# Kernel optimization log

Measured on AMD Instinct MI355X. Metric: run time of the kernel, lower is better.

The kernel has to match this reference:

```python
import jax, jax.numpy as jnp
import numpy as np

N_BITS = 8
QMAX = 2 ** (N_BITS - 1) - 1  # 127 for int8 symmetric
EPS = 1e-8


def fake_quant(x, axis):
    """Symmetric per-slice (row/col) dynamic fake quantization with STE-compatible form."""
    amax = jnp.max(jnp.abs(x), axis=axis, keepdims=True)
    scale = jnp.maximum(amax, EPS) / QMAX
    q = jnp.clip(jnp.round(x / scale), -QMAX - 1, QMAX) * scale
    return q


def setup_inputs() -> dict:
    key = jax.random.key(0)
    k1, k2 = jax.random.split(key)
    inputs1 = jax.random.normal(k1, (2, 16, 2048, 128), dtype=jnp.float32)
    inputs2 = jax.random.normal(k2, (2, 16, 128, 2048), dtype=jnp.float32)
    return {"inputs1": inputs1, "inputs2": inputs2}


def reference(inputs1, inputs2):
    # input1: row-wise (axes=-1) quant; input2: axes=-1 (module default); output: row-wise
    q1 = fake_quant(inputs1, axis=-1)
    q2 = fake_quant(inputs2, axis=-1)
    out = jnp.matmul(q1, q2)  # [B, H, S, S]
    return fake_quant(out, axis=-1)
```

## Files before the change

kernel.cpp:

```cpp
#include <hip/hip_runtime.h>
#include <hip/hip_bf16.h>
#include <cstdint>

#define QMAXF 127.0f
#define EPSQ 1e-8f

typedef __bf16 bf16x8 __attribute__((ext_vector_type(8)));
typedef float f32x4 __attribute__((ext_vector_type(4)));

static constexpr int BB = 32;
static constexpr int MM = 2048;
static constexpr int KK = 128;
static constexpr int NN = 2048;

static constexpr size_t OFF_Q1   = 0;
static constexpr size_t OFF_Q2T  = OFF_Q1  + (size_t)BB*MM*KK*2;
static constexpr size_t OFF_S1   = OFF_Q2T + (size_t)BB*NN*KK*2;
static constexpr size_t OFF_S2   = OFF_S1  + (size_t)BB*MM*4;

__global__ __launch_bounds__(256) void quant_rows128(const float* __restrict__ x,
                                                     unsigned short* __restrict__ q,
                                                     float* __restrict__ s1) {
    int wave = threadIdx.x >> 6, lane = threadIdx.x & 63;
    int row = blockIdx.x * 4 + wave;
    const float2* xr = reinterpret_cast<const float2*>(x) + (size_t)row * 64;
    float2 v = xr[lane];
    float a = fmaxf(fabsf(v.x), fabsf(v.y));
#pragma unroll
    for (int m = 32; m; m >>= 1) a = fmaxf(a, __shfl_xor(a, m));
    float scale = fmaxf(a, EPSQ) / QMAXF;
    float i0 = fminf(fmaxf(rintf(v.x / scale), -128.f), 127.f);
    float i1 = fminf(fmaxf(rintf(v.y / scale), -128.f), 127.f);
    __bf16 h0 = (__bf16)i0, h1 = (__bf16)i1;
    ushort2 st;
    st.x = *reinterpret_cast<unsigned short*>(&h0);
    st.y = *reinterpret_cast<unsigned short*>(&h1);
    reinterpret_cast<ushort2*>(q + (size_t)row * 128)[lane ^ ((row & 7) << 2)] = st;
    if (lane == 0) s1[row] = scale;
}

__global__ __launch_bounds__(256) void amax_rows2048(const float* __restrict__ x,
                                                     float* __restrict__ s2) {
    int row = blockIdx.x;
    const float4* xr = reinterpret_cast<const float4*>(x) + (size_t)row * 512;
    int t = threadIdx.x;
    float4 v0 = xr[t], v1 = xr[t + 256];
    float a = fmaxf(fmaxf(fmaxf(fabsf(v0.x), fabsf(v0.y)), fmaxf(fabsf(v0.z), fabsf(v0.w))),
                    fmaxf(fmaxf(fabsf(v1.x), fabsf(v1.y)), fmaxf(fabsf(v1.z), fabsf(v1.w))));
#pragma unroll
    for (int m = 32; m; m >>= 1) a = fmaxf(a, __shfl_xor(a, m));
    __shared__ float red[4];
    if ((t & 63) == 0) red[t >> 6] = a;
    __syncthreads();
    if (t == 0) {
        float m0 = fmaxf(fmaxf(red[0], red[1]), fmaxf(red[2], red[3]));
        s2[row] = fmaxf(m0, EPSQ) / QMAXF;
    }
}

__global__ __launch_bounds__(256) void quant_transpose(const float* __restrict__ x,
                                                       const float* __restrict__ s2,
                                                       unsigned short* __restrict__ q2t) {
    int b = blockIdx.x >> 5;
    int n0 = (blockIdx.x & 31) * 64;
    __shared__ unsigned short lds[64][136];
    int t = threadIdx.x;
    int rr = t >> 4, cc = t & 15;
#pragma unroll
    for (int p = 0; p < 8; ++p) {
        int k = p * 16 + rr;
        float s = s2[b * 128 + k];
        const float4* src = reinterpret_cast<const float4*>(x + ((size_t)b * 128 + k) * 2048 + n0);
        float4 v = src[cc];
        float f[4] = {v.x, v.y, v.z, v.w};
#pragma unroll
        for (int e = 0; e < 4; ++e) {
            float iq = fminf(fmaxf(rintf(f[e] / s), -128.f), 127.f);
            __bf16 h = (__bf16)(iq * s);
            lds[cc * 4 + e][k] = *reinterpret_cast<unsigned short*>(&h);
        }
    }
    __syncthreads();
    int nl = t >> 2, seg = t & 3;
    int sw = nl & 7;
    uint4* dstrow = reinterpret_cast<uint4*>(q2t + ((size_t)b * 2048 + n0 + nl) * 128);
#pragma unroll
    for (int j = 0; j < 4; ++j)
        dstrow[(seg * 4 + j) ^ sw] = *reinterpret_cast<const uint4*>(&lds[nl][seg * 32 + j * 8]);
}

__global__ __launch_bounds__(256, 2) void gemm_fused(const unsigned short* __restrict__ qa,
                                                     const unsigned short* __restrict__ qbt,
                                                     const float* __restrict__ s1,
                                                     float* __restrict__ out) {
    int id = blockIdx.x;
    int nid = (id & 7) * 64 + (id >> 3);
    int b = nid >> 4, mt = nid & 15;

    __shared__ unsigned short Bt[2][16384];
    __shared__ float rowAmax[128], sOsc[128], sQs[128], sS1[128];

    int tid = threadIdx.x, wave = tid >> 6, lane = tid & 63;
    if (tid < 128) {
        rowAmax[tid] = 0.f;
        sS1[tid] = s1[b * 2048 + mt * 128 + tid];
    }

    {
        const char* Ag = (const char*)(qa + (size_t)(b * 16 + mt) * 16384);
        const char* Bg = (const char*)(qbt + (size_t)(b * 16) * 16384);
        char* lA = (char*)&Bt[1][0];
        char* lB = (char*)&Bt[0][0];
#pragma unroll
        for (int i = 0; i < 8; ++i) {
            int off = i * 4096 + wave * 1024;
            __builtin_amdgcn_global_load_lds(
                (const __attribute__((address_space(1))) uint32_t*)(Ag + off + lane * 16),
                (__attribute__((address_space(3))) uint32_t*)(lA + off), 16, 0, 0);
            __builtin_amdgcn_global_load_lds(
                (const __attribute__((address_space(1))) uint32_t*)(Bg + off + lane * 16),
                (__attribute__((address_space(3))) uint32_t*)(lB + off), 16, 0, 0);
        }
    }
    __syncthreads();

    int wm = wave >> 1, wn = wave & 1;
    int lr = lane & 15, lg = lane >> 4;
    int swz = (lr & 7) << 3;

    bf16x8 afr[4][4];
#pragma unroll
    for (int ks = 0; ks < 4; ++ks)
#pragma unroll
        for (int mi = 0; mi < 4; ++mi)
            afr[ks][mi] = *reinterpret_cast<const bf16x8*>(
                &Bt[1][(wm * 64 + mi * 16 + lr) * 128 + ((ks * 32 + lg * 8) ^ swz)]);
    __syncthreads();

    size_t ob = (size_t)b * 2048 * 2048;
    float rmax[4] = {0.f, 0.f, 0.f, 0.f};

    for (int it = 0; it < 16; ++it) {
        int cur = it & 1;
        if (it < 15) {
            const char* Bg = (const char*)(qbt + (size_t)(b * 16 + it + 1) * 16384);
            char* lB = (char*)&Bt[cur ^ 1][0];
#pragma unroll
            for (int i = 0; i < 8; ++i) {
                int off = i * 4096 + wave * 1024;
                __builtin_amdgcn_global_load_lds(
                    (const __attribute__((address_space(1))) uint32_t*)(Bg + off + lane * 16),
                    (__attribute__((address_space(3))) uint32_t*)(lB + off), 16, 0, 0);
            }
        }

        f32x4 acc[4][4];
#pragma unroll
        for (int mi = 0; mi < 4; ++mi)
#pragma unroll
            for (int ni = 0; ni < 4; ++ni) {
                f32x4 z = {0.f, 0.f, 0.f, 0.f};
                acc[mi][ni] = z;
            }
#pragma unroll
        for (int ks = 0; ks < 4; ++ks) {
            int kb = (ks * 32 + lg * 8) ^ swz;
            bf16x8 bfr[4];
#pragma unroll
            for (int ni = 0; ni < 4; ++ni)
                bfr[ni] = *reinterpret_cast<const bf16x8*>(&Bt[cur][(wn * 64 + ni * 16 + lr) * 128 + kb]);
#pragma unroll
            for (int mi = 0; mi < 4; ++mi)
#pragma unroll
                for (int ni = 0; ni < 4; ++ni)
                    acc[mi][ni] = __builtin_amdgcn_mfma_f32_16x16x32_bf16(bfr[ni], afr[ks][mi], acc[mi][ni], 0, 0, 0);
        }
#pragma unroll
        for (int mi = 0; mi < 4; ++mi)
#pragma unroll
            for (int ni = 0; ni < 4; ++ni)
#pragma unroll
                for (int r = 0; r < 4; ++r)
                    rmax[mi] = fmaxf(rmax[mi], fabsf(acc[mi][ni][r]));
        __syncthreads();
    }

#pragma unroll
    for (int mi = 0; mi < 4; ++mi) {
        float v = rmax[mi];
        v = fmaxf(v, __shfl_xor(v, 16));
        v = fmaxf(v, __shfl_xor(v, 32));
        if (lg == 0) {
            int row = wm * 64 + mi * 16 + lr;
            atomicMax(reinterpret_cast<unsigned*>(&rowAmax[row]), __float_as_uint(v));
        }
    }
    __syncthreads();
    if (tid < 128) {
        float am = rowAmax[tid] * sS1[tid];
        float osc = fmaxf(am, EPSQ) / QMAXF;
        sOsc[tid] = osc;
        sQs[tid] = sS1[tid] / osc;
    }
    __syncthreads();

    const unsigned short* Bimg = qbt + (size_t)b * 16 * 16384;
    for (int nt = 0; nt < 16; ++nt) {
        f32x4 acc[4][4];
#pragma unroll
        for (int mi = 0; mi < 4; ++mi)
#pragma unroll
            for (int ni = 0; ni < 4; ++ni) {
                f32x4 z = {0.f, 0.f, 0.f, 0.f};
                acc[mi][ni] = z;
            }
#pragma unroll
        for (int ks = 0; ks < 4; ++ks) {
            int kb = (ks * 32 + lg * 8) ^ swz;
            bf16x8 bfr[4];
#pragma unroll
            for (int ni = 0; ni < 4; ++ni)
                bfr[ni] = *reinterpret_cast<const bf16x8*>(
                    &Bimg[(size_t)(nt * 128 + wn * 64 + ni * 16 + lr) * 128 + kb]);
#pragma unroll
            for (int mi = 0; mi < 4; ++mi)
#pragma unroll
                for (int ni = 0; ni < 4; ++ni)
                    acc[mi][ni] = __builtin_amdgcn_mfma_f32_16x16x32_bf16(bfr[ni], afr[ks][mi], acc[mi][ni], 0, 0, 0);
        }
#pragma unroll
        for (int mi = 0; mi < 4; ++mi) {
            int row = wm * 64 + mi * 16 + lr;
            float qs = sQs[row], osc = sOsc[row];
            size_t rowoff = ob + (size_t)(mt * 128 + row) * 2048 + nt * 128 + wn * 64 + lg * 4;
#pragma unroll
            for (int ni = 0; ni < 4; ++ni) {
                f32x4 qv;
                qv[0] = fminf(fmaxf(rintf(acc[mi][ni][0] * qs), -128.f), 127.f) * osc;
                qv[1] = fminf(fmaxf(rintf(acc[mi][ni][1] * qs), -128.f), 127.f) * osc;
                qv[2] = fminf(fmaxf(rintf(acc[mi][ni][2] * qs), -128.f), 127.f) * osc;
                qv[3] = fminf(fmaxf(rintf(acc[mi][ni][3] * qs), -128.f), 127.f) * osc;
                *reinterpret_cast<f32x4*>(&out[rowoff + ni * 16]) = qv;
            }
        }
    }
}

extern "C" void kernel_launch(void* const* d_in, const int* in_sizes, int n_in,
                              void* d_out, int out_size, void* d_ws, size_t ws_size,
                              hipStream_t stream) {
    const float* in1 = (const float*)d_in[0];
    const float* in2 = (const float*)d_in[1];
    char* ws = (char*)d_ws;
    unsigned short* q1  = (unsigned short*)(ws + OFF_Q1);
    unsigned short* q2t = (unsigned short*)(ws + OFF_Q2T);
    float* s1   = (float*)(ws + OFF_S1);
    float* s2   = (float*)(ws + OFF_S2);
    float* out  = (float*)d_out;

    quant_rows128 <<<BB * MM / 4, 256, 0, stream>>>(in1, q1, s1);
    amax_rows2048 <<<BB * KK,     256, 0, stream>>>(in2, s2);
    quant_transpose<<<BB * (NN / 64), 256, 0, stream>>>(in2, s2, q2t);
    gemm_fused    <<<BB * 16,     256, 0, stream>>>(q1, q2t, s1, out);
}
```

Measured before the change: 220.8 us.

## Drop LDS staging and register-prefetch next B tile from global in both passes

Removes the shared-memory double buffer and global_load_lds path for A and B. A fragments are now read directly from global into registers, and B fragments for the next N tile are prefetched into registers while the current tile's MFMAs run, in both the amax pass and the quantize-write pass. This removes the per-iteration __syncthreads and frees a large amount of LDS. In exchange it raises VGPR pressure (a 4x4 bf16x8 prefetch buffer), which may hurt occupancy under launch_bounds(256,2), and it relies on uncoalesced global/L2 fragment loads instead of LDS.

Measured after the change: 191.8 us, median of 2. 1.15x faster.

```diff
diff --git a/kernel.cpp b/kernel.cpp
--- a/kernel.cpp
+++ b/kernel.cpp
@@ -97,7 +97,6 @@
     int nid = (id & 7) * 64 + (id >> 3);
     int b = nid >> 4, mt = nid & 15;
 
-    __shared__ unsigned short Bt[2][16384];
     __shared__ float rowAmax[128], sOsc[128], sQs[128], sS1[128];
 
     int tid = threadIdx.x, wave = tid >> 6, lane = tid & 63;
@@ -106,54 +105,38 @@
         sS1[tid] = s1[b * 2048 + mt * 128 + tid];
     }
 
-    {
-        const char* Ag = (const char*)(qa + (size_t)(b * 16 + mt) * 16384);
-        const char* Bg = (const char*)(qbt + (size_t)(b * 16) * 16384);
-        char* lA = (char*)&Bt[1][0];
-        char* lB = (char*)&Bt[0][0];
-#pragma unroll
-        for (int i = 0; i < 8; ++i) {
-            int off = i * 4096 + wave * 1024;
-            __builtin_amdgcn_global_load_lds(
-                (const __attribute__((address_space(1))) uint32_t*)(Ag + off + lane * 16),
-                (__attribute__((address_space(3))) uint32_t*)(lA + off), 16, 0, 0);
-            __builtin_amdgcn_global_load_lds(
-                (const __attribute__((address_space(1))) uint32_t*)(Bg + off + lane * 16),
-                (__attribute__((address_space(3))) uint32_t*)(lB + off), 16, 0, 0);
-        }
-    }
-    __syncthreads();
-
     int wm = wave >> 1, wn = wave & 1;
     int lr = lane & 15, lg = lane >> 4;
     int swz = (lr & 7) << 3;
 
     bf16x8 afr[4][4];
+    {
+        const unsigned short* Ai = qa + (size_t)(b * 16 + mt) * 16384;
+#pragma unroll
+        for (int ks = 0; ks < 4; ++ks)
+#pragma unroll
+            for (int mi = 0; mi < 4; ++mi)
+                afr[ks][mi] = *reinterpret_cast<const bf16x8*>(
+                    &Ai[(wm * 64 + mi * 16 + lr) * 128 + ((ks * 32 + lg * 8) ^ swz)]);
+    }
+
+    const unsigned short* Bimg = qbt + (size_t)b * 16 * 16384;
+    auto boff = [&](int nt, int ks, int ni) -> size_t {
+        return (size_t)(nt * 128 + wn * 64 + ni * 16 + lr) * 128 + ((ks * 32 + lg * 8) ^ swz);
+    };
+
+    bf16x8 bfr[4][4];
 #pragma unroll
     for (int ks = 0; ks < 4; ++ks)
 #pragma unroll
-        for (int mi = 0; mi < 4; ++mi)
-            afr[ks][mi] = *reinterpret_cast<const bf16x8*>(
-                &Bt[1][(wm * 64 + mi * 16 + lr) * 128 + ((ks * 32 + lg * 8) ^ swz)]);
-    __syncthreads();
+        for (int ni = 0; ni < 4; ++ni)
+            bfr[ks][ni] = *reinterpret_cast<const bf16x8*>(&Bimg[boff(0, ks, ni)]);
 
     size_t ob = (size_t)b * 2048 * 2048;
     float rmax[4] = {0.f, 0.f, 0.f, 0.f};
 
-    for (int it = 0; it < 16; ++it) {
-        int cur = it & 1;
-        if (it < 15) {
-            const char* Bg = (const char*)(qbt + (size_t)(b * 16 + it + 1) * 16384);
-            char* lB = (char*)&Bt[cur ^ 1][0];
-#pragma unroll
-            for (int i = 0; i < 8; ++i) {
-                int off = i * 4096 + wave * 1024;
-                __builtin_amdgcn_global_load_lds(
-                    (const __attribute__((address_space(1))) uint32_t*)(Bg + off + lane * 16),
-                    (__attribute__((address_space(3))) uint32_t*)(lB + off), 16, 0, 0);
-            }
-        }
-
+    for (int nt = 0; nt < 16; ++nt) {
+        int nn = (nt + 1) & 15;
         f32x4 acc[4][4];
 #pragma unroll
         for (int mi = 0; mi < 4; ++mi)
@@ -164,16 +147,14 @@
             }
 #pragma unroll
         for (int ks = 0; ks < 4; ++ks) {
-            int kb = (ks * 32 + lg * 8) ^ swz;
-            bf16x8 bfr[4];
+#pragma unroll
+            for (int mi = 0; mi < 4; ++mi)
+#pragma unroll
+                for (int ni = 0; ni < 4; ++ni)
+                    acc[mi][ni] = __builtin_amdgcn_mfma_f32_16x16x32_bf16(bfr[ks][ni], afr[ks][mi], acc[mi][ni], 0, 0, 0);
 #pragma unroll
             for (int ni = 0; ni < 4; ++ni)
-                bfr[ni] = *reinterpret_cast<const bf16x8*>(&Bt[cur][(wn * 64 + ni * 16 + lr) * 128 + kb]);
-#pragma unroll
-            for (int mi = 0; mi < 4; ++mi)
-#pragma unroll
-                for (int ni = 0; ni < 4; ++ni)
-                    acc[mi][ni] = __builtin_amdgcn_mfma_f32_16x16x32_bf16(bfr[ni], afr[ks][mi], acc[mi][ni], 0, 0, 0);
+                bfr[ks][ni] = *reinterpret_cast<const bf16x8*>(&Bimg[boff(nn, ks, ni)]);
         }
 #pragma unroll
         for (int mi = 0; mi < 4; ++mi)
@@ -182,7 +163,6 @@
 #pragma unroll
                 for (int r = 0; r < 4; ++r)
                     rmax[mi] = fmaxf(rmax[mi], fabsf(acc[mi][ni][r]));
-        __syncthreads();
     }
 
 #pragma unroll
@@ -204,8 +184,8 @@
     }
     __syncthreads();
 
-    const unsigned short* Bimg = qbt + (size_t)b * 16 * 16384;
     for (int nt = 0; nt < 16; ++nt) {
+        int nn = (nt + 1) & 15;
         f32x4 acc[4][4];
 #pragma unroll
         for (int mi = 0; mi < 4; ++mi)
@@ -216,17 +196,14 @@
             }
 #pragma unroll
         for (int ks = 0; ks < 4; ++ks) {
-            int kb = (ks * 32 + lg * 8) ^ swz;
-            bf16x8 bfr[4];
+#pragma unroll
+            for (int mi = 0; mi < 4; ++mi)
+#pragma unroll
+                for (int ni = 0; ni < 4; ++ni)
+                    acc[mi][ni] = __builtin_amdgcn_mfma_f32_16x16x32_bf16(bfr[ks][ni], afr[ks][mi], acc[mi][ni], 0, 0, 0);
 #pragma unroll
             for (int ni = 0; ni < 4; ++ni)
-                bfr[ni] = *reinterpret_cast<const bf16x8*>(
-                    &Bimg[(size_t)(nt * 128 + wn * 64 + ni * 16 + lr) * 128 + kb]);
-#pragma unroll
-            for (int mi = 0; mi < 4; ++mi)
-#pragma unroll
-                for (int ni = 0; ni < 4; ++ni)
-                    acc[mi][ni] = __builtin_amdgcn_mfma_f32_16x16x32_bf16(bfr[ni], afr[ks][mi], acc[mi][ni], 0, 0, 0);
+                bfr[ks][ni] = *reinterpret_cast<const bf16x8*>(&Bimg[boff(nn, ks, ni)]);
         }
 #pragma unroll
         for (int mi = 0; mi < 4; ++mi) {
```
